# Optimization experiments

Hardware: AMD Instinct MI355X
Metric: run time of the kernel (lower is better)

## Reference

```python
import jax, jax.numpy as jnp
import numpy as np

B, C, H, W = 2, 128, 64, 64
N, R = 16, 4            # d_state, dt_rank = ceil(128/32)
R2 = 2 * R
Ch = C // 2
Cout = 128
L = H * W
EPS_LN = 1e-6
EPS_BN = 1e-5


def _ln_cf(x, w, b):
    # channels_first LayerNorm over dim 1
    u = x.mean(1, keepdims=True)
    s = ((x - u) ** 2).mean(1, keepdims=True)
    return w[None, :, None, None] * (x - u) / jnp.sqrt(s + EPS_LN) + b[None, :, None, None]


def _conv1x1(x, w, b):
    return jnp.einsum('bchw,oc->bohw', x, w) + b[None, :, None, None]


def _dwconv(x, w, b):
    out = jax.lax.conv_general_dilated(x, w, (1, 1), 'SAME',
        dimension_numbers=('NCHW', 'OIHW', 'NCHW'), feature_group_count=x.shape[1])
    return out + b[None, :, None, None]


def _selective_scan(u, delta, A, Bs, Cs, D):
    # u, delta: [B,L,C]; A: [C,N]; Bs, Cs: [B,L,N]; D: [C]
    dA = jnp.exp(delta[..., None] * A)                   # [B,L,C,N]
    dBu = (delta * u)[..., None] * Bs[:, :, None, :]     # [B,L,C,N]
    def step(h, xs):
        a, b = xs
        h = a * h + b
        return h, h
    h0 = jnp.zeros((u.shape[0], u.shape[2], A.shape[1]), u.dtype)
    _, hs = jax.lax.scan(step, h0, (jnp.moveaxis(dA, 1, 0), jnp.moveaxis(dBu, 1, 0)))
    hs = jnp.moveaxis(hs, 0, 1)                          # [B,L,C,N]
    return jnp.einsum('blcn,bln->blc', hs, Cs) + u * D


def _branch_ssm(x, xp_w, xp_b, dt_w, dt_b, A_log, Dp, reverse):
    b_, c_, h_, w_ = x.shape
    u = x.reshape(b_, c_, -1).transpose(0, 2, 1)         # [B,L,C/2]
    if reverse:
        u = u[:, ::-1]
    dbl = u @ xp_w.T + xp_b
    dt, Bs, Cs = jnp.split(dbl, [R, R + N], axis=-1)
    delta = jax.nn.softplus(dt @ dt_w.T + dt_b)
    y = _selective_scan(u, delta, -jnp.exp(A_log), Bs, Cs, Dp)
    if reverse:
        y = y[:, ::-1]
    return y.transpose(0, 2, 1).reshape(b_, c_, h_, w_)


def _sid_ssm(x, sorted_idx, xp_w, xp_b, dt_w, dt_b, A_log, Dp):
    b_, c_, h_, w_ = x.shape
    u = x.reshape(b_, c_, -1).transpose(0, 2, 1)         # [B,L,C]
    u = jnp.take_along_axis(u, sorted_idx[:, :, None], axis=1)
    dbl = u @ xp_w.T + xp_b
    dt, Bs, Cs = jnp.split(dbl, [R2, R2 + N], axis=-1)
    delta = jax.nn.softplus(dt @ dt_w.T + dt_b)
    y = _selective_scan(u, delta, -jnp.exp(A_log), Bs, Cs, Dp)
    inv = jnp.argsort(sorted_idx, axis=1)                # inverse permutation
    y = jnp.take_along_axis(y, inv[:, :, None], axis=1)
    return y.transpose(0, 2, 1).reshape(b_, c_, h_, w_)


def _forward(x, mask_fg, mask_bg, mask_uc,
             norm_in_w, norm_in_b, in_proj_w, in_proj_b,
             ln_mamba_w, ln_mamba_b, conv_mamba_w, conv_mamba_b,
             conv_res_w, conv_res_b,
             xproj_f_w, xproj_f_b, dtproj_f_w, dtproj_f_b, A_log_f, D_f,
             xproj_b_w, xproj_b_b, dtproj_b_w, dtproj_b_b, A_log_b, D_b,
             xproj_s_w, xproj_s_b, dtproj_s_w, dtproj_s_b, A_log_s, D_s,
             ln_cat_w, ln_cat_b,
             g0_w, g0_b, bn_g, bn_be, bn_m, bn_v, g1_w, g1_b,
             out_w, out_b, norm_out_w, norm_out_b):
    x = _ln_cf(x, norm_in_w, norm_in_b)
    xp = _conv1x1(x, in_proj_w, in_proj_b)               # [B,2C,H,W]
    x_mamba, x_res = xp[:, :C], xp[:, C:]
    x_mamba = _ln_cf(x_mamba, ln_mamba_w, ln_mamba_b)
    x_mamba = jax.nn.silu(_dwconv(x_mamba, conv_mamba_w, conv_mamba_b))
    x_res = jax.nn.silu(_dwconv(x_res, conv_res_w, conv_res_b))
    xf, xb = x_mamba[:, :Ch], x_mamba[:, Ch:]
    y_f = _branch_ssm(xf, xproj_f_w, xproj_f_b, dtproj_f_w, dtproj_f_b, A_log_f, D_f, False)
    y_b = _branch_ssm(xb, xproj_b_w, xproj_b_b, dtproj_b_w, dtproj_b_b, A_log_b, D_b, True)
    concat = _ln_cf(jnp.concatenate([y_f, y_b], 1), ln_cat_w, ln_cat_b)
    # SID priority ordering: fg > bg > uc > rest, ties broken by raster index
    fg = (mask_fg > 0.5).astype(x.dtype)
    bg = (mask_bg > 0.5).astype(x.dtype) * (1 - fg)
    uc = (mask_uc > 0.5).astype(x.dtype) * (1 - fg) * (1 - bg)
    prio = (fg * 3 + bg * 2 + uc).reshape(x.shape[0], -1) \
        + jnp.arange(L, dtype=x.dtype)[None] * 1e-4
    sorted_idx = jnp.argsort(-prio, axis=1)
    sid = _sid_ssm(x_mamba, sorted_idx, xproj_s_w, xproj_s_b, dtproj_s_w, dtproj_s_b, A_log_s, D_s)
    # gated fusion (BatchNorm in eval mode with running stats)
    g = _conv1x1(jnp.concatenate([concat, sid], 1), g0_w, g0_b)
    g = (g - bn_m[None, :, None, None]) / jnp.sqrt(bn_v + EPS_BN)[None, :, None, None]
    g = jax.nn.relu(g * bn_g[None, :, None, None] + bn_be[None, :, None, None])
    g = jax.nn.sigmoid(_conv1x1(g, g1_w, g1_b))
    fused = g * sid + (1 - g) * concat
    out = _conv1x1(jnp.concatenate([fused, x_res], 1), out_w, out_b)
    return _ln_cf(out, norm_out_w, norm_out_b)


def setup_inputs():
    keys = iter(jax.random.split(jax.random.key(0), 64))
    def rn(shape, s=1.0):
        return jax.random.normal(next(keys), shape, jnp.float32) * s
    def dt_bias(ch):
        dt = jnp.exp(jax.random.uniform(next(keys), (ch,)) * (np.log(0.1) - np.log(0.001)) + np.log(0.001))
        return dt + jnp.log(-jnp.expm1(-dt))  # inverse-softplus init as in torch code
    def a_log(ch):
        return jnp.log(jnp.tile(jnp.arange(1, N + 1, dtype=jnp.float32), (ch, 1)))
    s = 0.05
    return dict(
        x=rn((B, C, H, W)),
        mask_fg=jax.random.uniform(next(keys), (B, 1, H, W)),
        mask_bg=jax.random.uniform(next(keys), (B, 1, H, W)),
        mask_uc=jax.random.uniform(next(keys), (B, 1, H, W)),
        norm_in_w=jnp.ones((C,)), norm_in_b=jnp.zeros((C,)),
        in_proj_w=rn((2 * C, C), s), in_proj_b=jnp.zeros((2 * C,)),
        ln_mamba_w=jnp.ones((C,)), ln_mamba_b=jnp.zeros((C,)),
        conv_mamba_w=rn((C, 1, 3, 3), 0.2), conv_mamba_b=jnp.zeros((C,)),
        conv_res_w=rn((C, 1, 3, 3), 0.2), conv_res_b=jnp.zeros((C,)),
        xproj_f_w=rn((R + 2 * N, Ch), s), xproj_f_b=jnp.zeros((R + 2 * N,)),
        dtproj_f_w=rn((Ch, R), 0.5), dtproj_f_b=dt_bias(Ch),
        A_log_f=a_log(Ch), D_f=jnp.ones((Ch,)),
        xproj_b_w=rn((R + 2 * N, Ch), s), xproj_b_b=jnp.zeros((R + 2 * N,)),
        dtproj_b_w=rn((Ch, R), 0.5), dtproj_b_b=dt_bias(Ch),
        A_log_b=a_log(Ch), D_b=jnp.ones((Ch,)),
        xproj_s_w=rn((R2 + 2 * N, C), s), xproj_s_b=jnp.zeros((R2 + 2 * N,)),
        dtproj_s_w=rn((C, R2), 0.35), dtproj_s_b=dt_bias(C),
        A_log_s=a_log(C), D_s=jnp.ones((C,)),
        ln_cat_w=jnp.ones((C,)), ln_cat_b=jnp.zeros((C,)),
        g0_w=rn((C, 2 * C), s), g0_b=jnp.zeros((C,)),
        bn_g=jnp.ones((C,)), bn_be=jnp.zeros((C,)),
        bn_m=jnp.zeros((C,)), bn_v=jnp.ones((C,)),
        g1_w=rn((C, C), s), g1_b=jnp.zeros((C,)),
        out_w=rn((Cout, 2 * C), s), out_b=jnp.zeros((Cout,)),
        norm_out_w=jnp.ones((Cout,)), norm_out_b=jnp.zeros((Cout,)),
    )


def reference(x, mask_fg, mask_bg, mask_uc,
              norm_in_w, norm_in_b, in_proj_w, in_proj_b,
              ln_mamba_w, ln_mamba_b, conv_mamba_w, conv_mamba_b,
              conv_res_w, conv_res_b,
              xproj_f_w, xproj_f_b, dtproj_f_w, dtproj_f_b, A_log_f, D_f,
              xproj_b_w, xproj_b_b, dtproj_b_w, dtproj_b_b, A_log_b, D_b,
              xproj_s_w, xproj_s_b, dtproj_s_w, dtproj_s_b, A_log_s, D_s,
              ln_cat_w, ln_cat_b,
              g0_w, g0_b, bn_g, bn_be, bn_m, bn_v, g1_w, g1_b,
              out_w, out_b, norm_out_w, norm_out_b):
    return _forward(x, mask_fg, mask_bg, mask_uc,
                    norm_in_w, norm_in_b, in_proj_w, in_proj_b,
                    ln_mamba_w, ln_mamba_b, conv_mamba_w, conv_mamba_b,
                    conv_res_w, conv_res_b,
                    xproj_f_w, xproj_f_b, dtproj_f_w, dtproj_f_b, A_log_f, D_f,
                    xproj_b_w, xproj_b_b, dtproj_b_w, dtproj_b_b, A_log_b, D_b,
                    xproj_s_w, xproj_s_b, dtproj_s_w, dtproj_s_b, A_log_s, D_s,
                    ln_cat_w, ln_cat_b,
                    g0_w, g0_b, bn_g, bn_be, bn_m, bn_v, g1_w, g1_b,
                    out_w, out_b, norm_out_w, norm_out_b)
```

## Files before the change

### kernel.cpp

```cpp
#include <hip/hip_runtime.h>
#include <math.h>

#define Bn 2
#define Cn_ 128
#define Hn 64
#define Wn 64
#define Ln 4096
#define Nn 16

static constexpr float EPS_LN_C = 1e-6f;
static constexpr float EPS_BN_C = 1e-5f;

__device__ __forceinline__ float softplusf_(float x) {
    return fmaxf(x, 0.f) + log1pf(__expf(-fabsf(x)));
}
__device__ __forceinline__ float sigmoidf_(float x) {
    return 1.f / (1.f + __expf(-x));
}

template <int KSN>
__device__ __forceinline__ float4 sum_part4_(const float* __restrict__ p0, const float* __restrict__ p1,
                                             const float* __restrict__ p2, const float* __restrict__ p3,
                                             size_t e, float bias) {
    float4 a = *(const float4*)(p0 + e);
    if (KSN > 1) { float4 t = *(const float4*)(p1 + e); a.x += t.x; a.y += t.y; a.z += t.z; a.w += t.w; }
    if (KSN > 2) { float4 t = *(const float4*)(p2 + e); a.x += t.x; a.y += t.y; a.z += t.z; a.w += t.w; }
    if (KSN > 3) { float4 t = *(const float4*)(p3 + e); a.x += t.x; a.y += t.y; a.z += t.z; a.w += t.w; }
    a.x += bias; a.y += bias; a.z += bias; a.w += bias;
    return a;
}

__global__ __launch_bounds__(256) void ln_kernel(
    const float* __restrict__ inA, const float* __restrict__ inB, int csA,
    const float* __restrict__ lw, const float* __restrict__ lb,
    float* __restrict__ out, int csOut) {
    int b = blockIdx.y;
    int lane = threadIdx.x & 63;
    int q = threadIdx.x >> 6;
    int px = blockIdx.x * 64 + lane;
    __shared__ float s_s[4][64], s_s2[4][64];
    __shared__ float s_m[64], s_r[64];
    float s = 0.f, s2 = 0.f;
#pragma unroll
    for (int i = 0; i < 32; i++) {
        int c = q * 32 + i;
        const float* ptr = (inB && c >= 64) ? (inB + ((size_t)b * 64 + (c - 64)) * Ln)
                                            : (inA + ((size_t)b * csA + c) * Ln);
        float v = ptr[px];
        s += v; s2 += v * v;
    }
    s_s[q][lane] = s; s_s2[q][lane] = s2;
    __syncthreads();
    if (q == 0) {
        float ts = s_s[0][lane] + s_s[1][lane] + s_s[2][lane] + s_s[3][lane];
        float t2 = s_s2[0][lane] + s_s2[1][lane] + s_s2[2][lane] + s_s2[3][lane];
        float m = ts / 128.f;
        float var = fmaxf(t2 / 128.f - m * m, 0.f);
        s_m[lane] = m; s_r[lane] = 1.f / sqrtf(var + EPS_LN_C);
    }
    __syncthreads();
    float m = s_m[lane], r = s_r[lane];
#pragma unroll
    for (int i = 0; i < 32; i++) {
        int c = q * 32 + i;
        const float* ptr = (inB && c >= 64) ? (inB + ((size_t)b * 64 + (c - 64)) * Ln)
                                            : (inA + ((size_t)b * csA + c) * Ln);
        float v = ptr[px];
        out[((size_t)b * csOut + c) * Ln + px] = (v - m) * r * lw[c] + lb[c];
    }
}

__global__ __launch_bounds__(256) void combine_ln_kernel(
    const float* __restrict__ p0, const float* __restrict__ p1,
    const float* __restrict__ p2, const float* __restrict__ p3,
    const float* __restrict__ bias,
    const float* __restrict__ lw, const float* __restrict__ lb,
    float* __restrict__ out) {
    int b = blockIdx.y;
    int lane = threadIdx.x & 63;
    int q = threadIdx.x >> 6;
    int px = blockIdx.x * 64 + lane;
    __shared__ float s_s[4][64], s_s2[4][64];
    __shared__ float s_m[64], s_r[64];
    float v[32];
    float s = 0.f, s2 = 0.f;
#pragma unroll
    for (int i = 0; i < 32; i++) {
        int c = q * 32 + i;
        size_t e = ((size_t)b * 128 + c) * Ln + px;
        float a = p0[e] + p1[e] + p2[e] + p3[e] + bias[c];
        v[i] = a; s += a; s2 += a * a;
    }
    s_s[q][lane] = s; s_s2[q][lane] = s2;
    __syncthreads();
    if (q == 0) {
        float ts = s_s[0][lane] + s_s[1][lane] + s_s[2][lane] + s_s[3][lane];
        float t2 = s_s2[0][lane] + s_s2[1][lane] + s_s2[2][lane] + s_s2[3][lane];
        float m = ts / 128.f;
        float var = fmaxf(t2 / 128.f - m * m, 0.f);
        s_m[lane] = m; s_r[lane] = 1.f / sqrtf(var + EPS_LN_C);
    }
    __syncthreads();
    float m = s_m[lane], r = s_r[lane];
#pragma unroll
    for (int i = 0; i < 32; i++) {
        int c = q * 32 + i;
        out[((size_t)b * 128 + c) * Ln + px] = (v[i] - m) * r * lw[c] + lb[c];
    }
}

__global__ __launch_bounds__(256) void conv1x1_kernel(
    const float* __restrict__ inA, const float* __restrict__ inB,
    int cinA, int csA, int cinB, int csB, int cout, int csOut,
    const float* __restrict__ w, const float* __restrict__ wB,
    const float* __restrict__ bias, const float* __restrict__ biasB, long inAoffB,
    const float* __restrict__ bng, const float* __restrict__ bnbe,
    const float* __restrict__ bnm, const float* __restrict__ bnv,
    int epilogue, float* __restrict__ out,
    int ksn, int kchunk,
    float* __restrict__ p0, float* __restrict__ p1,
    float* __restrict__ p2, float* __restrict__ p3, long pbrOff) {
    int z = blockIdx.z;
    int br = 0, b = z;
    if (z >= Bn) { br = 1; b = z - Bn; }
    int ks = 0, og = blockIdx.y;
    if (ksn > 1) { ks = blockIdx.y % ksn; og = blockIdx.y / ksn; }
    int o0 = og * 4;
    int k0 = ks * kchunk;
    int CL = kchunk;
    int cin = cinA + cinB;
    const float* wsel = br ? wB : w;
    const float* bsel = br ? biasB : bias;
    const float* wrow[4];
#pragma unroll
    for (int j = 0; j < 4; j++)
        wrow[j] = wsel + (size_t)min(o0 + j, cout - 1) * cin + k0;
    int l = (blockIdx.x * 256 + threadIdx.x) * 4;
    const float* src;
    if (k0 < cinA) src = inA + (br ? inAoffB : 0) + ((size_t)b * csA + k0) * Ln + l;
    else           src = inB + ((size_t)b * csB + (k0 - cinA)) * Ln + l;
    float4 acc[4];
#pragma unroll
    for (int j = 0; j < 4; j++) {
        float bj = (ksn > 1) ? 0.f : bsel[min(o0 + j, cout - 1)];
        acc[j] = make_float4(bj, bj, bj, bj);
    }
    float4 v0[4], v1[4];
#define CLD(V, c0_) do { _Pragma("unroll") for (int j_ = 0; j_ < 4; ++j_) \
        V[j_] = *(const float4*)(src + (size_t)((c0_) + j_) * Ln); } while (0)
#define CFM(V, c0_) do { _Pragma("unroll") for (int j_ = 0; j_ < 4; ++j_) { \
        _Pragma("unroll") for (int o_ = 0; o_ < 4; ++o_) { \
            float wv_ = wrow[o_][(c0_) + j_]; \
            acc[o_].x = fmaf(wv_, V[j_].x, acc[o_].x); \
            acc[o_].y = fmaf(wv_, V[j_].y, acc[o_].y); \
            acc[o_].z = fmaf(wv_, V[j_].z, acc[o_].z); \
            acc[o_].w = fmaf(wv_, V[j_].w, acc[o_].w); } } } while (0)
    CLD(v0, 0);
    for (int cc = 0; cc < CL; cc += 8) {
        CLD(v1, cc + 4);
        CFM(v0, cc);
        if (cc + 8 < CL) CLD(v0, cc + 8);
        CFM(v1, cc + 4);
    }
#undef CLD
#undef CFM
    if (ksn > 1) {
        float* pp = (ks == 0) ? p0 : (ks == 1) ? p1 : (ks == 2) ? p2 : p3;
        if (br) pp += pbrOff;
#pragma unroll
        for (int j = 0; j < 4; j++) {
            int o = o0 + j;
            if (o >= cout) continue;
            *(float4*)(pp + ((size_t)b * cout + o) * Ln + l) = acc[j];
        }
    } else {
#pragma unroll
        for (int j = 0; j < 4; j++) {
            int o = o0 + j;
            if (o >= cout) continue;
            float4 v = acc[j];
            if (epilogue == 1) {
                float sc = (1.f / sqrtf(bnv[o] + EPS_BN_C)) * bng[o];
                float sh = bnbe[o] - bnm[o] * sc;
                v.x = fmaxf(fmaf(v.x, sc, sh), 0.f);
                v.y = fmaxf(fmaf(v.y, sc, sh), 0.f);
                v.z = fmaxf(fmaf(v.z, sc, sh), 0.f);
                v.w = fmaxf(fmaf(v.w, sc, sh), 0.f);
            } else if (epilogue == 2) {
                v.x = sigmoidf_(v.x); v.y = sigmoidf_(v.y);
                v.z = sigmoidf_(v.z); v.w = sigmoidf_(v.w);
            }
            *(float4*)(out + ((size_t)b * csOut + o) * Ln + l) = v;
        }
    }
}

__global__ __launch_bounds__(256) void combine_kernel(
    const float* __restrict__ p0, const float* __restrict__ p1,
    const float* __restrict__ p2, const float* __restrict__ p3, int ksn,
    const float* __restrict__ bias,
    const float* __restrict__ bng, const float* __restrict__ bnbe,
    const float* __restrict__ bnm, const float* __restrict__ bnv,
    int epilogue, float* __restrict__ out, int cout, int n4) {
    int i = blockIdx.x * 256 + threadIdx.x;
    if (i >= n4) return;
    size_t e = (size_t)i * 4;
    int o = (int)((e / Ln) % cout);
    float4 a = *(const float4*)(p0 + e);
    if (ksn > 1) { float4 t = *(const float4*)(p1 + e); a.x += t.x; a.y += t.y; a.z += t.z; a.w += t.w; }
    if (epilogue != 3) {
        if (ksn > 2) { float4 t = *(const float4*)(p2 + e); a.x += t.x; a.y += t.y; a.z += t.z; a.w += t.w; }
        if (ksn > 3) { float4 t = *(const float4*)(p3 + e); a.x += t.x; a.y += t.y; a.z += t.z; a.w += t.w; }
    }
    float bj = bias[o];
    a.x += bj; a.y += bj; a.z += bj; a.w += bj;
    if (epilogue == 1) {
        float sc = (1.f / sqrtf(bnv[o] + EPS_BN_C)) * bng[o];
        float sh = bnbe[o] - bnm[o] * sc;
        a.x = fmaxf(fmaf(a.x, sc, sh), 0.f);
        a.y = fmaxf(fmaf(a.y, sc, sh), 0.f);
        a.z = fmaxf(fmaf(a.z, sc, sh), 0.f);
        a.w = fmaxf(fmaf(a.w, sc, sh), 0.f);
    } else if (epilogue == 2) {
        a.x = sigmoidf_(a.x); a.y = sigmoidf_(a.y);
        a.z = sigmoidf_(a.z); a.w = sigmoidf_(a.w);
    } else if (epilogue == 3) {
        float4 s = *(const float4*)(p2 + e);
        float4 c = *(const float4*)(p3 + e);
        float g;
        g = sigmoidf_(a.x); a.x = g * s.x + (1.f - g) * c.x;
        g = sigmoidf_(a.y); a.y = g * s.y + (1.f - g) * c.y;
        g = sigmoidf_(a.z); a.z = g * s.z + (1.f - g) * c.z;
        g = sigmoidf_(a.w); a.w = g * s.w + (1.f - g) * c.w;
    }
    *(float4*)(out + e) = a;
}

__global__ void dwconv_kernel(const float* __restrict__ xmn, const float* __restrict__ xp,
                              const float* __restrict__ wm, const float* __restrict__ bm,
                              const float* __restrict__ wr, const float* __restrict__ brr,
                              float* __restrict__ xm, float* __restrict__ xr) {
    int b = blockIdx.z;
    int c2 = blockIdx.y;
    int l = blockIdx.x * blockDim.x + threadIdx.x;
    int h = l >> 6, w = l & 63;
    bool mamba = (c2 < 128);
    const float* in = mamba ? (xmn + ((size_t)b * 128 + c2) * Ln)
                            : (xp + ((size_t)b * 256 + c2) * Ln);
    const float* wt = mamba ? (wm + c2 * 9) : (wr + (c2 - 128) * 9);
    float acc = mamba ? bm[c2] : brr[c2 - 128];
#pragma unroll
    for (int dh = -1; dh <= 1; dh++) {
#pragma unroll
        for (int dw = -1; dw <= 1; dw++) {
            int hh = h + dh, ww = w + dw;
            if (hh < 0 || hh > 63 || ww < 0 || ww > 63) continue;
            acc = fmaf(in[hh * 64 + ww], wt[(dh + 1) * 3 + (dw + 1)], acc);
        }
    }
    float o = acc * sigmoidf_(acc);
    if (mamba) xm[((size_t)b * 128 + c2) * Ln + l] = o;
    else       xr[((size_t)b * 128 + (c2 - 128)) * Ln + l] = o;
}

__global__ __launch_bounds__(1024) void sort_kernel(const float* __restrict__ mfg,
                                                    const float* __restrict__ mbg,
                                                    const float* __restrict__ muc,
                                                    int* __restrict__ sidx) {
    int b = blockIdx.x;
    int t = threadIdx.x;
    const int PT = 4;
    __shared__ unsigned int wsum0[16], wsum1[16];
    __shared__ unsigned int tot01s, tot23s;

    int cls[PT];
    unsigned int c01 = 0, c23 = 0;
#pragma unroll
    for (int q = 0; q < PT; q++) {
        int j = t * PT + q;
        int i = Ln - 1 - j;
        float f = mfg[b * Ln + i], g = mbg[b * Ln + i], u = muc[b * Ln + i];
        int k = (f > 0.5f) ? 3 : (g > 0.5f) ? 2 : (u > 0.5f) ? 1 : 0;
        cls[q] = k;
        if (k == 0) c01 += 1u;
        else if (k == 1) c01 += (1u << 16);
        else if (k == 2) c23 += 1u;
        else c23 += (1u << 16);
    }
    unsigned int s01 = c01, s23 = c23;
    int lane = t & 63;
    for (int d = 1; d < 64; d <<= 1) {
        unsigned int o01 = __shfl_up(s01, (unsigned)d, 64);
        unsigned int o23 = __shfl_up(s23, (unsigned)d, 64);
        if (lane >= d) { s01 += o01; s23 += o23; }
    }
    int wid = t >> 6;
    if (lane == 63) { wsum0[wid] = s01; wsum1[wid] = s23; }
    __syncthreads();
    if (t == 0) {
        unsigned int a0 = 0, a1 = 0;
        for (int k2 = 0; k2 < 16; k2++) {
            unsigned int v0 = wsum0[k2], v1 = wsum1[k2];
            wsum0[k2] = a0; wsum1[k2] = a1;
            a0 += v0; a1 += v1;
        }
        tot01s = a0; tot23s = a1;
    }
    __syncthreads();
    unsigned int ex01 = s01 - c01 + wsum0[wid];
    unsigned int ex23 = s23 - c23 + wsum1[wid];
    unsigned int cnt1 = tot01s >> 16;
    unsigned int cnt2 = tot23s & 0xffffu, cnt3 = tot23s >> 16;
    unsigned int off3 = 0, off2 = cnt3, off1 = cnt3 + cnt2, off0 = cnt3 + cnt2 + cnt1;
    unsigned int run0 = ex01 & 0xffffu, run1 = ex01 >> 16;
    unsigned int run2 = ex23 & 0xffffu, run3 = ex23 >> 16;
#pragma unroll
    for (int q = 0; q < PT; q++) {
        int j = t * PT + q;
        int i = Ln - 1 - j;
        int k = cls[q];
        unsigned int pos;
        if (k == 0) pos = off0 + run0++;
        else if (k == 1) pos = off1 + run1++;
        else if (k == 2) pos = off2 + run2++;
        else pos = off3 + run3++;
        sidx[b * Ln + pos] = i;
    }
}

__global__ __launch_bounds__(256) void gather_kernel(const float* __restrict__ xm,
                                                     const int* __restrict__ sidx,
                                                     float* __restrict__ us) {
    int b = blockIdx.z;
    int c = blockIdx.y;
    int t = blockIdx.x * 256 + threadIdx.x;
    int pix = sidx[b * Ln + t];
    us[((size_t)b * 128 + c) * Ln + t] = xm[((size_t)b * 128 + c) * Ln + pix];
}

template <int R, int NQ, int KSN, int NBR>
__global__ __launch_bounds__(256) void delta_pack_fused(
    const float* __restrict__ q0, const float* __restrict__ q1,
    const float* __restrict__ q2, const float* __restrict__ q3,
    long brOff, int RT,
    const float* __restrict__ xbF, const float* __restrict__ xbB,
    const float* __restrict__ dtwF, const float* __restrict__ dtbF,
    const float* __restrict__ dtwB, const float* __restrict__ dtbB,
    float* __restrict__ dpkF, float* __restrict__ dpkB) {
    int z = blockIdx.z;
    int br = (NBR > 1) ? (z >> 1) : 0;
    int b  = (NBR > 1) ? (z & 1) : z;
    long off = br ? brOff : 0;
    const float* p0 = q0 + off;
    const float* p1 = (KSN > 1) ? q1 + off : nullptr;
    const float* p2 = (KSN > 2) ? q2 + off : nullptr;
    const float* p3 = (KSN > 3) ? q3 + off : nullptr;
    const float* xb  = br ? xbB  : xbF;
    const float* dtw = br ? dtwB : dtwF;
    const float* dtb = br ? dtbB : dtbF;
    float* dpk = br ? dpkB : dpkF;

    int cq = blockIdx.y;
    int tq = blockIdx.x * 64 + (threadIdx.x >> 2);
    int clow = threadIdx.x & 3;
    int c = cq * 4 + clow;
    int t0 = tq * 4;
    float4 a[R];
#pragma unroll
    for (int r = 0; r < R; r++)
        a[r] = sum_part4_<KSN>(p0, p1, p2, p3, ((size_t)b * RT + r) * Ln + t0, xb[r]);
    float bj = dtb[c];
    float4 acc = make_float4(bj, bj, bj, bj);
#pragma unroll
    for (int r = 0; r < R; r++) {
        float wv = dtw[c * R + r];
        acc.x = fmaf(wv, a[r].x, acc.x);
        acc.y = fmaf(wv, a[r].y, acc.y);
        acc.z = fmaf(wv, a[r].z, acc.z);
        acc.w = fmaf(wv, a[r].w, acc.w);
    }
    float4 o;
    o.x = softplusf_(acc.x); o.y = softplusf_(acc.y);
    o.z = softplusf_(acc.z); o.w = softplusf_(acc.w);
    *(float4*)(dpk + (((size_t)b * NQ + cq) * 1024 + tq) * 16 + clow * 4) = o;
}

template <int KSN, int NBR>
__global__ __launch_bounds__(256) void pack_bc_fused(
    const float* __restrict__ q0, const float* __restrict__ q1,
    const float* __restrict__ q2, const float* __restrict__ q3,
    long brOff, int RT, int rB, int rC,
    const float* __restrict__ xbF, const float* __restrict__ xbB,
    float* __restrict__ dBF, float* __restrict__ dCF,
    float* __restrict__ dBB, float* __restrict__ dCB) {
    int br = (NBR > 1) ? (int)blockIdx.z : 0;
    int b = blockIdx.y;
    long off = br ? brOff : 0;
    const float* p0 = q0 + off;
    const float* p1 = (KSN > 1) ? q1 + off : nullptr;
    const float* p2 = (KSN > 2) ? q2 + off : nullptr;
    const float* p3 = (KSN > 3) ? q3 + off : nullptr;
    const float* xb = br ? xbB : xbF;
    float* dB = br ? dBB : dBF;
    float* dC = br ? dCB : dCF;

    int idx = blockIdx.x * 256 + threadIdx.x;
    int tb = idx >> 4, n = idx & 15;
    float4 vB = sum_part4_<KSN>(p0, p1, p2, p3, ((size_t)b * RT + rB + n) * Ln + tb * 4, xb[rB + n]);
    float4 vC = sum_part4_<KSN>(p0, p1, p2, p3, ((size_t)b * RT + rC + n) * Ln + tb * 4, xb[rC + n]);
    *(float4*)(dB + ((size_t)b * 1024 + tb) * 64 + n * 4) = vB;
    *(float4*)(dC + ((size_t)b * 1024 + tb) * 64 + n * 4) = vC;
}

#define NCHUNK 128
#define CG 2

#define DPPADD(p) do { \
    p += __int_as_float(__builtin_amdgcn_update_dpp(0, __float_as_int(p), 0xB1, 0xF, 0xF, true)); \
    p += __int_as_float(__builtin_amdgcn_update_dpp(0, __float_as_int(p), 0x4E, 0xF, 0xF, true)); \
    p += __int_as_float(__builtin_amdgcn_update_dpp(0, __float_as_int(p), 0x124, 0xF, 0xF, true)); \
    p += __int_as_float(__builtin_amdgcn_update_dpp(0, __float_as_int(p), 0x128, 0xF, 0xF, true)); \
} while (0)

template <int REV>
__device__ __forceinline__ void p1_chunk(const float* __restrict__ up, const float* __restrict__ dp,
                                         const float* __restrict__ bp, float A, int c0,
                                         float& hout, float& Pout) {
    float h = 0.f, P = 1.f;
    float4 U0[4], D0[4], B0[4], U1[4], D1[4], B1[4];
#define PHYS1(ci) (REV ? (255 - (ci)) : (ci))
#define LOAD1(U, D, Bb, ci) do { int pb_ = PHYS1(ci) * 16; int tb_ = PHYS1(ci) * 4; \
    _Pragma("unroll") for (int j_ = 0; j_ < 4; ++j_) { \
        U[j_]  = *(const float4*)(up + pb_ + 4 * j_); \
        D[j_]  = *(const float4*)(dp + (size_t)(tb_ + j_) * 16); \
        Bb[j_] = *(const float4*)(bp + (size_t)(tb_ + j_) * 64); \
    } } while (0)
#define STEP1(u_, d_, B_) do { float a_ = __expf((d_) * A); h = fmaf(a_, h, (d_) * (u_) * (B_)); P *= a_; } while (0)
#define COMP1(U, D, Bb) do { \
    if (!REV) { _Pragma("unroll") for (int j_ = 0; j_ < 4; ++j_) { \
        STEP1(U[j_].x, D[j_].x, Bb[j_].x); STEP1(U[j_].y, D[j_].y, Bb[j_].y); \
        STEP1(U[j_].z, D[j_].z, Bb[j_].z); STEP1(U[j_].w, D[j_].w, Bb[j_].w); } } \
    else { _Pragma("unroll") for (int j_ = 3; j_ >= 0; --j_) { \
        STEP1(U[j_].w, D[j_].w, Bb[j_].w); STEP1(U[j_].z, D[j_].z, Bb[j_].z); \
        STEP1(U[j_].y, D[j_].y, Bb[j_].y); STEP1(U[j_].x, D[j_].x, Bb[j_].x); } } } while (0)
    LOAD1(U0, D0, B0, c0);
    for (int it = 0; it < CG; it += 2) {
        LOAD1(U1, D1, B1, c0 + it + 1);
        COMP1(U0, D0, B0);
        if (it + 2 < CG) LOAD1(U0, D0, B0, c0 + it + 2);
        COMP1(U1, D1, B1);
    }
    hout = h; Pout = P;
#undef PHYS1
#undef LOAD1
#undef STEP1
#undef COMP1
}

__global__ __launch_bounds__(64) void scan_p1_kernel(
    const float* __restrict__ xm, const float* __restrict__ us,
    const float* __restrict__ dfpk, const float* __restrict__ bpkf, const float* __restrict__ Alf,
    const float* __restrict__ dbpk, const float* __restrict__ bpkb, const float* __restrict__ Alb,
    const float* __restrict__ dspk, const float* __restrict__ bpks, const float* __restrict__ Als,
    float* __restrict__ hf, float* __restrict__ Pp) {
    int g = blockIdx.x, k = blockIdx.y;
    int lane = threadIdx.x;
    int n = lane & 15, cl = lane >> 4;
    int c0 = k * CG;
    float h, P;
    if (g < 32) {
        int b = g >> 4, cg = g & 15, c = cg * 4 + cl;
        float A = -__expf(Alf[c * 16 + n]);
        p1_chunk<0>(xm + ((size_t)b * 128 + c) * Ln,
                    dfpk + (((size_t)b * 16 + cg) * 1024) * 16 + cl * 4,
                    bpkf + (size_t)b * 65536 + n * 4, A, c0, h, P);
    } else if (g < 64) {
        int g2 = g - 32, b = g2 >> 4, cg = g2 & 15, c = cg * 4 + cl;
        float A = -__expf(Alb[c * 16 + n]);
        p1_chunk<1>(xm + ((size_t)b * 128 + 64 + c) * Ln,
                    dbpk + (((size_t)b * 16 + cg) * 1024) * 16 + cl * 4,
                    bpkb + (size_t)b * 65536 + n * 4, A, c0, h, P);
    } else {
        int g2 = g - 64, b = g2 >> 5, cg = g2 & 31, c = cg * 4 + cl;
        float A = -__expf(Als[c * 16 + n]);
        p1_chunk<0>(us + ((size_t)b * 128 + c) * Ln,
                    dspk + (((size_t)b * 32 + cg) * 1024) * 16 + cl * 4,
                    bpks + (size_t)b * 65536 + n * 4, A, c0, h, P);
    }
    int o = (g * NCHUNK + k) * 64 + lane;
    hf[o] = h; Pp[o] = P;
}

__global__ void scan_stitch_kernel(float* __restrict__ hf, const float* __restrict__ Pp) {
    int id = blockIdx.x * blockDim.x + threadIdx.x;
    int g = id >> 6, lane = id & 63;
    float h = 0.f;
    for (int kb = 0; kb < NCHUNK / 8; kb++) {
        float P8[8], H8[8];
#pragma unroll
        for (int j = 0; j < 8; j++) {
            int o = (g * NCHUNK + kb * 8 + j) * 64 + lane;
            P8[j] = Pp[o]; H8[j] = hf[o];
        }
#pragma unroll
        for (int j = 0; j < 8; j++) {
            int o = (g * NCHUNK + kb * 8 + j) * 64 + lane;
            hf[o] = h;
            h = fmaf(P8[j], h, H8[j]);
        }
    }
}

#define STEPP(u_, d_, B_, C_) ({ \
    float dA_ = __expf((d_) * A); \
    h = fmaf(dA_, h, (d_) * (u_) * (B_)); \
    float p_ = h * (C_); \
    DPPADD(p_); \
    fmaf((u_), Dc, p_); })

template <int MODE>
__device__ __forceinline__ void p2_chunk(const float* __restrict__ up, const float* __restrict__ dp,
                                         const float* __restrict__ bp, const float* __restrict__ cp,
                                         const int* __restrict__ sp, float* __restrict__ yp,
                                         float A, float Dc, int n, int c0, float h) {
    constexpr bool REV = (MODE == 1);
    constexpr bool SIDM = (MODE == 2);
    float4 U0[4], D0[4], B0[4], C0[4], U1[4], D1[4], B1[4], C1[4];
    int4 I0[4] = {}, I1[4] = {};
#define PHYS(ci) (REV ? (255 - (ci)) : (ci))
#define LOADC(U, D, Bb, Cc, I, ci) do { int pb_ = PHYS(ci) * 16; int tb_ = PHYS(ci) * 4; \
    _Pragma("unroll") for (int j_ = 0; j_ < 4; ++j_) { \
        U[j_]  = *(const float4*)(up + pb_ + 4 * j_); \
        D[j_]  = *(const float4*)(dp + (size_t)(tb_ + j_) * 16); \
        Bb[j_] = *(const float4*)(bp + (size_t)(tb_ + j_) * 64); \
        Cc[j_] = *(const float4*)(cp + (size_t)(tb_ + j_) * 64); \
        if (SIDM) I[j_] = *(const int4*)(sp + pb_ + 4 * j_); \
    } } while (0)
#define COMPC(U, D, Bb, Cc, I, ci) do { int pb_ = PHYS(ci) * 16; \
    if (SIDM) { \
        _Pragma("unroll") for (int j_ = 0; j_ < 4; ++j_) { \
            float y0_ = STEPP(U[j_].x, D[j_].x, Bb[j_].x, Cc[j_].x); if (n == 0) yp[I[j_].x] = y0_; \
            float y1_ = STEPP(U[j_].y, D[j_].y, Bb[j_].y, Cc[j_].y); if (n == 0) yp[I[j_].y] = y1_; \
            float y2_ = STEPP(U[j_].z, D[j_].z, Bb[j_].z, Cc[j_].z); if (n == 0) yp[I[j_].z] = y2_; \
            float y3_ = STEPP(U[j_].w, D[j_].w, Bb[j_].w, Cc[j_].w); if (n == 0) yp[I[j_].w] = y3_; \
        } \
    } else if (!REV) { \
        _Pragma("unroll") for (int j_ = 0; j_ < 4; ++j_) { \
            float4 y4_; \
            y4_.x = STEPP(U[j_].x, D[j_].x, Bb[j_].x, Cc[j_].x); \
            y4_.y = STEPP(U[j_].y, D[j_].y, Bb[j_].y, Cc[j_].y); \
            y4_.z = STEPP(U[j_].z, D[j_].z, Bb[j_].z, Cc[j_].z); \
            y4_.w = STEPP(U[j_].w, D[j_].w, Bb[j_].w, Cc[j_].w); \
            if (n == 0) *(float4*)(yp + pb_ + 4 * j_) = y4_; \
        } \
    } else { \
        _Pragma("unroll") for (int j_ = 3; j_ >= 0; --j_) { \
            float4 y4_; \
            y4_.w = STEPP(U[j_].w, D[j_].w, Bb[j_].w, Cc[j_].w); \
            y4_.z = STEPP(U[j_].z, D[j_].z, Bb[j_].z, Cc[j_].z); \
            y4_.y = STEPP(U[j_].y, D[j_].y, Bb[j_].y, Cc[j_].y); \
            y4_.x = STEPP(U[j_].x, D[j_].x, Bb[j_].x, Cc[j_].x); \
            if (n == 0) *(float4*)(yp + pb_ + 4 * j_) = y4_; \
        } \
    } } while (0)
    LOADC(U0, D0, B0, C0, I0, c0);
    for (int it = 0; it < CG; it += 2) {
        LOADC(U1, D1, B1, C1, I1, c0 + it + 1);
        COMPC(U0, D0, B0, C0, I0, c0 + it);
        if (it + 2 < CG) LOADC(U0, D0, B0, C0, I0, c0 + it + 2);
        COMPC(U1, D1, B1, C1, I1, c0 + it + 1);
    }
#undef PHYS
#undef LOADC
#undef COMPC
}

__global__ __launch_bounds__(64) void scan_p2_kernel(
    const float* __restrict__ xm, const float* __restrict__ us,
    const float* __restrict__ dfpk, const float* __restrict__ bpkf, const float* __restrict__ cpkf,
    const float* __restrict__ Alf, const float* __restrict__ Dfp,
    const float* __restrict__ dbpk, const float* __restrict__ bpkb, const float* __restrict__ cpkb,
    const float* __restrict__ Alb, const float* __restrict__ Dbp,
    const float* __restrict__ dspk, const float* __restrict__ bpks, const float* __restrict__ cpks,
    const float* __restrict__ Als, const float* __restrict__ Dsp,
    const int* __restrict__ sidx, const float* __restrict__ hi,
    float* __restrict__ yf, float* __restrict__ yb, float* __restrict__ ys) {
    int g = blockIdx.x, k = blockIdx.y;
    int lane = threadIdx.x;
    int n = lane & 15, cl = lane >> 4;
    int c0 = k * CG;
    float h0 = hi[(g * NCHUNK + k) * 64 + lane];
    if (g < 32) {
        int b = g >> 4, cg = g & 15, c = cg * 4 + cl;
        float A = -__expf(Alf[c * 16 + n]);
        p2_chunk<0>(xm + ((size_t)b * 128 + c) * Ln,
                    dfpk + (((size_t)b * 16 + cg) * 1024) * 16 + cl * 4,
                    bpkf + (size_t)b * 65536 + n * 4, cpkf + (size_t)b * 65536 + n * 4,
                    nullptr, yf + ((size_t)b * 64 + c) * Ln, A, Dfp[c], n, c0, h0);
    } else if (g < 64) {
        int g2 = g - 32, b = g2 >> 4, cg = g2 & 15, c = cg * 4 + cl;
        float A = -__expf(Alb[c * 16 + n]);
        p2_chunk<1>(xm + ((size_t)b * 128 + 64 + c) * Ln,
                    dbpk + (((size_t)b * 16 + cg) * 1024) * 16 + cl * 4,
                    bpkb + (size_t)b * 65536 + n * 4, cpkb + (size_t)b * 65536 + n * 4,
                    nullptr, yb + ((size_t)b * 64 + c) * Ln, A, Dbp[c], n, c0, h0);
    } else {
        int g2 = g - 64, b = g2 >> 5, cg = g2 & 31, c = cg * 4 + cl;
        float A = -__expf(Als[c * 16 + n]);
        p2_chunk<2>(us + ((size_t)b * 128 + c) * Ln,
                    dspk + (((size_t)b * 32 + cg) * 1024) * 16 + cl * 4,
                    bpks + (size_t)b * 65536 + n * 4, cpks + (size_t)b * 65536 + n * 4,
                    sidx + b * Ln, ys + ((size_t)b * 128 + c) * Ln, A, Dsp[c], n, c0, h0);
    }
}

extern "C" void kernel_launch(void* const* d_in, const int* in_sizes, int n_in,
                              void* d_out, int out_size, void* d_ws, size_t ws_size,
                              hipStream_t stream) {
    const float* x    = (const float*)d_in[0];
    const float* mfg  = (const float*)d_in[1];
    const float* mbg  = (const float*)d_in[2];
    const float* muc  = (const float*)d_in[3];
    const float* niw  = (const float*)d_in[4];
    const float* nib  = (const float*)d_in[5];
    const float* inw  = (const float*)d_in[6];
    const float* inb  = (const float*)d_in[7];
    const float* lmw  = (const float*)d_in[8];
    const float* lmb  = (const float*)d_in[9];
    const float* cmw  = (const float*)d_in[10];
    const float* cmb  = (const float*)d_in[11];
    const float* crw  = (const float*)d_in[12];
    const float* crb  = (const float*)d_in[13];
    const float* xwf  = (const float*)d_in[14];
    const float* xbf  = (const float*)d_in[15];
    const float* dtwf = (const float*)d_in[16];
    const float* dtbf = (const float*)d_in[17];
    const float* Alf  = (const float*)d_in[18];
    const float* Dfp  = (const float*)d_in[19];
    const float* xwb  = (const float*)d_in[20];
    const float* xbb  = (const float*)d_in[21];
    const float* dtwb = (const float*)d_in[22];
    const float* dtbb = (const float*)d_in[23];
    const float* Alb  = (const float*)d_in[24];
    const float* Dbp  = (const float*)d_in[25];
    const float* xws  = (const float*)d_in[26];
    const float* xbs  = (const float*)d_in[27];
    const float* dtws = (const float*)d_in[28];
    const float* dtbs = (const float*)d_in[29];
    const float* Als  = (const float*)d_in[30];
    const float* Dsp  = (const float*)d_in[31];
    const float* lcw  = (const float*)d_in[32];
    const float* lcb  = (const float*)d_in[33];
    const float* g0w  = (const float*)d_in[34];
    const float* g0b  = (const float*)d_in[35];
    const float* bng  = (const float*)d_in[36];
    const float* bnbe = (const float*)d_in[37];
    const float* bnm  = (const float*)d_in[38];
    const float* bnv  = (const float*)d_in[39];
    const float* g1w  = (const float*)d_in[40];
    const float* g1b  = (const float*)d_in[41];
    const float* outw = (const float*)d_in[42];
    const float* outb = (const float*)d_in[43];
    const float* now  = (const float*)d_in[44];
    const float* nob  = (const float*)d_in[45];

    float* W = (float*)d_ws;
    const size_t R_XP = 0;
    const size_t R_A  = 2097152;
    const size_t R_B  = 4194304;
    const size_t R_N  = 6291456;
    const size_t R_XM = 7340032;
    const size_t R_XR = 8388608;
    const size_t R_US = 9437184;
    const size_t R_IDX= 10485760;
    const size_t XNORM = R_N, XP = R_XP, XMN = R_N;
    const size_t XPJ0 = R_XP, XPJ1 = R_XP + 294912;
    const size_t DFPK = R_N, DBPK = R_N + 524288, DSPK = R_B + 1048576;
    const size_t BPKF = R_A, CPKF = R_A + 131072, BPKB = R_A + 262144,
                 CPKB = R_A + 393216, BPKS = R_A + 524288, CPKS = R_A + 655360;
    const size_t XS0 = R_XP, XS1 = R_XP + 327680, XS2 = R_XP + 655360, XS3 = R_XP + 983040;
    const size_t HF = R_XP, PP = R_XP + 1048576;
    const size_t YF = R_A + 786432, YB = R_A + 1310720, YS = R_B;
    const size_t CATLN = R_N, FUSED = R_N;
    const size_t GBUF = R_XM;

    int* idxp = (int*)(W + R_IDX);
    dim3 blk(256);
    const float* nil = nullptr;

    ln_kernel<<<dim3(64, 2), blk, 0, stream>>>(x, nullptr, 128, niw, nib, W + XNORM, 128);
    conv1x1_kernel<<<dim3(4, 128, 2), blk, 0, stream>>>(
        W + XNORM, nullptr, 128, 128, 0, 0, 256, 256, inw, nullptr, inb, nullptr, 0,
        nil, nil, nil, nil, 0, nullptr, 2, 64, W + R_A, W + R_B, nullptr, nullptr, 0);
    combine_kernel<<<2048, blk, 0, stream>>>(
        W + R_A, W + R_B, nullptr, nullptr, 2, inb, nil, nil, nil, nil, 0, W + XP, 256, 524288);
    ln_kernel<<<dim3(64, 2), blk, 0, stream>>>(W + XP, nullptr, 256, lmw, lmb, W + XMN, 128);
    dwconv_kernel<<<dim3(16, 256, 2), blk, 0, stream>>>(
        W + XMN, W + XP, cmw, cmb, crw, crb, W + R_XM, W + R_XR);
    sort_kernel<<<2, 1024, 0, stream>>>(mfg, mbg, muc, idxp);
    conv1x1_kernel<<<dim3(4, 18, 4), blk, 0, stream>>>(
        W + R_XM, nullptr, 64, 128, 0, 0, 36, 36, xwf, xwb, xbf, xbb, (long)64 * Ln,
        nil, nil, nil, nil, 0, nullptr, 2, 32, W + XPJ0, W + XPJ1, nullptr, nullptr, (long)589824);
    delta_pack_fused<4, 16, 2, 2><<<dim3(16, 16, 4), blk, 0, stream>>>(
        W + XPJ0, W + XPJ1, nullptr, nullptr, (long)589824, 36,
        xbf, xbb, dtwf, dtbf, dtwb, dtbb, W + DFPK, W + DBPK);
    pack_bc_fused<2, 2><<<dim3(64, 2, 2), blk, 0, stream>>>(
        W + XPJ0, W + XPJ1, nullptr, nullptr, (long)589824, 36, 4, 20,
        xbf, xbb, W + BPKF, W + CPKF, W + BPKB, W + CPKB);
    gather_kernel<<<dim3(16, 128, 2), blk, 0, stream>>>(W + R_XM, idxp, W + R_US);
    conv1x1_kernel<<<dim3(4, 40, 2), blk, 0, stream>>>(
        W + R_US, nullptr, 128, 128, 0, 0, 40, 40, xws, nullptr, xbs, nullptr, 0,
        nil, nil, nil, nil, 0, nullptr, 4, 32, W + XS0, W + XS1, W + XS2, W + XS3, 0);
    delta_pack_fused<8, 32, 4, 1><<<dim3(16, 32, 2), blk, 0, stream>>>(
        W + XS0, W + XS1, W + XS2, W + XS3, 0, 40,
        xbs, nullptr, dtws, dtbs, nullptr, nullptr, W + DSPK, nullptr);
    pack_bc_fused<4, 1><<<dim3(64, 2, 1), blk, 0, stream>>>(
        W + XS0, W + XS1, W + XS2, W + XS3, 0, 40, 8, 24,
        xbs, nullptr, W + BPKS, W + CPKS, nullptr, nullptr);
    scan_p1_kernel<<<dim3(128, NCHUNK), 64, 0, stream>>>(
        W + R_XM, W + R_US,
        W + DFPK, W + BPKF, Alf,
        W + DBPK, W + BPKB, Alb,
        W + DSPK, W + BPKS, Als,
        W + HF, W + PP);
    scan_stitch_kernel<<<32, 256, 0, stream>>>(W + HF, W + PP);
    scan_p2_kernel<<<dim3(128, NCHUNK), 64, 0, stream>>>(
        W + R_XM, W + R_US,
        W + DFPK, W + BPKF, W + CPKF, Alf, Dfp,
        W + DBPK, W + BPKB, W + CPKB, Alb, Dbp,
        W + DSPK, W + BPKS, W + CPKS, Als, Dsp,
        idxp, W + HF, W + YF, W + YB, W + YS);
    ln_kernel<<<dim3(64, 2), blk, 0, stream>>>(W + YF, W + YB, 64, lcw, lcb, W + CATLN, 128);
    conv1x1_kernel<<<dim3(4, 128, 2), blk, 0, stream>>>(
        W + CATLN, W + YS, 128, 128, 128, 128, 128, 128, g0w, nullptr, g0b, nullptr, 0,
        nil, nil, nil, nil, 0, nullptr, 4, 64,
        W + R_A, W + R_A + 1048576, W + R_XP, W + R_XP + 1048576, 0);
    combine_kernel<<<1024, blk, 0, stream>>>(
        W + R_A, W + R_A + 1048576, W + R_XP, W + R_XP + 1048576, 4, g0b,
        bng, bnbe, bnm, bnv, 1, W + GBUF, 128, 262144);
    conv1x1_kernel<<<dim3(4, 64, 2), blk, 0, stream>>>(
        W + GBUF, nullptr, 128, 128, 0, 0, 128, 128, g1w, nullptr, g1b, nullptr, 0,
        nil, nil, nil, nil, 0, nullptr, 2, 64, W + R_A, W + R_A + 1048576, nullptr, nullptr, 0);
    combine_kernel<<<1024, blk, 0, stream>>>(
        W + R_A, W + R_A + 1048576, W + YS, W + CATLN, 2, g1b,
        nil, nil, nil, nil, 3, W + FUSED, 128, 262144);
    conv1x1_kernel<<<dim3(4, 128, 2), blk, 0, stream>>>(
        W + FUSED, W + R_XR, 128, 128, 128, 128, 128, 128, outw, nullptr, outb, nullptr, 0,
        nil, nil, nil, nil, 0, nullptr, 4, 64,
        W + R_A, W + R_A + 1048576, W + R_XP, W + R_XP + 1048576, 0);
    combine_ln_kernel<<<dim3(64, 2), blk, 0, stream>>>(
        W + R_A, W + R_A + 1048576, W + R_XP, W + R_XP + 1048576, outb, now, nob,
        (float*)d_out);
}
```

Before: 216.2 us.

## Fuse input LayerNorm into in_proj conv1x1 via precomputed per-pixel stats

The input LayerNorm no longer writes a full normalized tensor. A new stats kernel writes only per-pixel mean and rstd, and the in_proj 1x1 conv applies the normalization to each input value as it is loaded. The in_proj conv also drops its two-way K-split (ksn=1, kchunk=128), so it writes its output directly and the separate combine kernel is no longer needed. This removes a full-tensor write and read plus one launch, but halves the in_proj grid and adds per-load normalization arithmetic.

```diff
diff --git a/kernel.cpp b/kernel.cpp
--- a/kernel.cpp
+++ b/kernel.cpp
@@ -28,6 +28,33 @@
     if (KSN > 3) { float4 t = *(const float4*)(p3 + e); a.x += t.x; a.y += t.y; a.z += t.z; a.w += t.w; }
     a.x += bias; a.y += bias; a.z += bias; a.w += bias;
     return a;
+}
+
+__global__ __launch_bounds__(256) void ln_stats_kernel(
+    const float* __restrict__ in, int csA,
+    float* __restrict__ mean, float* __restrict__ rstd) {
+    int b = blockIdx.y;
+    int lane = threadIdx.x & 63;
+    int q = threadIdx.x >> 6;
+    int px = blockIdx.x * 64 + lane;
+    __shared__ float s_s[4][64], s_s2[4][64];
+    float s = 0.f, s2 = 0.f;
+#pragma unroll
+    for (int i = 0; i < 32; i++) {
+        int c = q * 32 + i;
+        float v = in[((size_t)b * csA + c) * Ln + px];
+        s += v; s2 += v * v;
+    }
+    s_s[q][lane] = s; s_s2[q][lane] = s2;
+    __syncthreads();
+    if (q == 0) {
+        float ts = s_s[0][lane] + s_s[1][lane] + s_s[2][lane] + s_s[3][lane];
+        float t2 = s_s2[0][lane] + s_s2[1][lane] + s_s2[2][lane] + s_s2[3][lane];
+        float m = ts / 128.f;
+        float var = fmaxf(t2 / 128.f - m * m, 0.f);
+        mean[b * Ln + px] = m;
+        rstd[b * Ln + px] = 1.f / sqrtf(var + EPS_LN_C);
+    }
 }
 
 __global__ __launch_bounds__(256) void ln_kernel(
@@ -114,6 +141,8 @@
     int cinA, int csA, int cinB, int csB, int cout, int csOut,
     const float* __restrict__ w, const float* __restrict__ wB,
     const float* __restrict__ bias, const float* __restrict__ biasB, long inAoffB,
+    const float* __restrict__ lnm, const float* __restrict__ lnr,
+    const float* __restrict__ lnw, const float* __restrict__ lnb,
     const float* __restrict__ bng, const float* __restrict__ bnbe,
     const float* __restrict__ bnm, const float* __restrict__ bnv,
     int epilogue, float* __restrict__ out,
@@ -139,6 +168,12 @@
     const float* src;
     if (k0 < cinA) src = inA + (br ? inAoffB : 0) + ((size_t)b * csA + k0) * Ln + l;
     else           src = inB + ((size_t)b * csB + (k0 - cinA)) * Ln + l;
+    bool ln = (lnw != nullptr);
+    float4 m4 = make_float4(0, 0, 0, 0), r4 = make_float4(0, 0, 0, 0);
+    if (ln) {
+        m4 = *(const float4*)(lnm + (size_t)b * Ln + l);
+        r4 = *(const float4*)(lnr + (size_t)b * Ln + l);
+    }
     float4 acc[4];
 #pragma unroll
     for (int j = 0; j < 4; j++) {
@@ -146,8 +181,14 @@
         acc[j] = make_float4(bj, bj, bj, bj);
     }
     float4 v0[4], v1[4];
-#define CLD(V, c0_) do { _Pragma("unroll") for (int j_ = 0; j_ < 4; ++j_) \
-        V[j_] = *(const float4*)(src + (size_t)((c0_) + j_) * Ln); } while (0)
+#define CLD(V, c0_) do { _Pragma("unroll") for (int j_ = 0; j_ < 4; ++j_) { \
+        V[j_] = *(const float4*)(src + (size_t)((c0_) + j_) * Ln); \
+        if (ln) { float lwv_ = lnw[k0 + (c0_) + j_], lb2_ = lnb[k0 + (c0_) + j_]; \
+            V[j_].x = fmaf((V[j_].x - m4.x) * r4.x, lwv_, lb2_); \
+            V[j_].y = fmaf((V[j_].y - m4.y) * r4.y, lwv_, lb2_); \
+            V[j_].z = fmaf((V[j_].z - m4.z) * r4.z, lwv_, lb2_); \
+            V[j_].w = fmaf((V[j_].w - m4.w) * r4.w, lwv_, lb2_); } \
+    } } while (0)
 #define CFM(V, c0_) do { _Pragma("unroll") for (int j_ = 0; j_ < 4; ++j_) { \
         _Pragma("unroll") for (int o_ = 0; o_ < 4; ++o_) { \
             float wv_ = wrow[o_][(c0_) + j_]; \
@@ -673,7 +714,8 @@
     const size_t R_XR = 8388608;
     const size_t R_US = 9437184;
     const size_t R_IDX= 10485760;
-    const size_t XNORM = R_N, XP = R_XP, XMN = R_N;
+    const size_t XP = R_XP, XMN = R_N;
+    const size_t MEAN0 = R_A, RSTD0 = R_A + 8192;
     const size_t XPJ0 = R_XP, XPJ1 = R_XP + 294912;
     const size_t DFPK = R_N, DBPK = R_N + 524288, DSPK = R_B + 1048576;
     const size_t BPKF = R_A, CPKF = R_A + 131072, BPKB = R_A + 262144,
@@ -688,18 +730,18 @@
     dim3 blk(256);
     const float* nil = nullptr;
 
-    ln_kernel<<<dim3(64, 2), blk, 0, stream>>>(x, nullptr, 128, niw, nib, W + XNORM, 128);
-    conv1x1_kernel<<<dim3(4, 128, 2), blk, 0, stream>>>(
-        W + XNORM, nullptr, 128, 128, 0, 0, 256, 256, inw, nullptr, inb, nullptr, 0,
-        nil, nil, nil, nil, 0, nullptr, 2, 64, W + R_A, W + R_B, nullptr, nullptr, 0);
-    combine_kernel<<<2048, blk, 0, stream>>>(
-        W + R_A, W + R_B, nullptr, nullptr, 2, inb, nil, nil, nil, nil, 0, W + XP, 256, 524288);
+    ln_stats_kernel<<<dim3(64, 2), blk, 0, stream>>>(x, 128, W + MEAN0, W + RSTD0);
+    conv1x1_kernel<<<dim3(4, 64, 2), blk, 0, stream>>>(
+        x, nullptr, 128, 128, 0, 0, 256, 256, inw, nullptr, inb, nullptr, 0,
+        W + MEAN0, W + RSTD0, niw, nib,
+        nil, nil, nil, nil, 0, W + XP, 1, 128, nullptr, nullptr, nullptr, nullptr, 0);
     ln_kernel<<<dim3(64, 2), blk, 0, stream>>>(W + XP, nullptr, 256, lmw, lmb, W + XMN, 128);
     dwconv_kernel<<<dim3(16, 256, 2), blk, 0, stream>>>(
         W + XMN, W + XP, cmw, cmb, crw, crb, W + R_XM, W + R_XR);
     sort_kernel<<<2, 1024, 0, stream>>>(mfg, mbg, muc, idxp);
     conv1x1_kernel<<<dim3(4, 18, 4), blk, 0, stream>>>(
         W + R_XM, nullptr, 64, 128, 0, 0, 36, 36, xwf, xwb, xbf, xbb, (long)64 * Ln,
+        nil, nil, nil, nil,
         nil, nil, nil, nil, 0, nullptr, 2, 32, W + XPJ0, W + XPJ1, nullptr, nullptr, (long)589824);
     delta_pack_fused<4, 16, 2, 2><<<dim3(16, 16, 4), blk, 0, stream>>>(
         W + XPJ0, W + XPJ1, nullptr, nullptr, (long)589824, 36,
@@ -710,6 +752,7 @@
     gather_kernel<<<dim3(16, 128, 2), blk, 0, stream>>>(W + R_XM, idxp, W + R_US);
     conv1x1_kernel<<<dim3(4, 40, 2), blk, 0, stream>>>(
         W + R_US, nullptr, 128, 128, 0, 0, 40, 40, xws, nullptr, xbs, nullptr, 0,
+        nil, nil, nil, nil,
         nil, nil, nil, nil, 0, nullptr, 4, 32, W + XS0, W + XS1, W + XS2, W + XS3, 0);
     delta_pack_fused<8, 32, 4, 1><<<dim3(16, 32, 2), blk, 0, stream>>>(
         W + XS0, W + XS1, W + XS2, W + XS3, 0, 40,
@@ -733,6 +776,7 @@
     ln_kernel<<<dim3(64, 2), blk, 0, stream>>>(W + YF, W + YB, 64, lcw, lcb, W + CATLN, 128);
     conv1x1_kernel<<<dim3(4, 128, 2), blk, 0, stream>>>(
         W + CATLN, W + YS, 128, 128, 128, 128, 128, 128, g0w, nullptr, g0b, nullptr, 0,
+        nil, nil, nil, nil,
         nil, nil, nil, nil, 0, nullptr, 4, 64,
         W + R_A, W + R_A + 1048576, W + R_XP, W + R_XP + 1048576, 0);
     combine_kernel<<<1024, blk, 0, stream>>>(
@@ -740,12 +784,14 @@
         bng, bnbe, bnm, bnv, 1, W + GBUF, 128, 262144);
     conv1x1_kernel<<<dim3(4, 64, 2), blk, 0, stream>>>(
         W + GBUF, nullptr, 128, 128, 0, 0, 128, 128, g1w, nullptr, g1b, nullptr, 0,
+        nil, nil, nil, nil,
         nil, nil, nil, nil, 0, nullptr, 2, 64, W + R_A, W + R_A + 1048576, nullptr, nullptr, 0);
     combine_kernel<<<1024, blk, 0, stream>>>(
         W + R_A, W + R_A + 1048576, W + YS, W + CATLN, 2, g1b,
         nil, nil, nil, nil, 3, W + FUSED, 128, 262144);
     conv1x1_kernel<<<dim3(4, 128, 2), blk, 0, stream>>>(
         W + FUSED, W + R_XR, 128, 128, 128, 128, 128, 128, outw, nullptr, outb, nullptr, 0,
+        nil, nil, nil, nil,
         nil, nil, nil, nil, 0, nullptr, 4, 64,
         W + R_A, W + R_A + 1048576, W + R_XP, W + R_XP + 1048576, 0);
     combine_ln_kernel<<<dim3(64, 2), blk, 0, stream>>>(
```

Measured after the change: 242.2 us. +12.0%, slower.
